# Performance work log

Hardware: AMD Instinct MI355X
Metric: run time of the kernel (lower is better)

Reference implementation:

```python
import jax, jax.numpy as jnp
import numpy as np

B, S, D = 8, 1024, 128
EPS = 1e-7
LN_EPS = 1e-3  # keras LayerNormalization default


def setup_inputs() -> dict:
    key = jax.random.key(0)
    ks = jax.random.split(key, 8)
    sd = 1.0 / np.sqrt(D)
    return {
        "x": jax.random.normal(ks[0], (B, S, D), jnp.float32),
        "Wq": jax.random.normal(ks[1], (D, D), jnp.float32) * sd,
        "bq": jnp.zeros((D,), jnp.float32),
        "Wm": jax.random.normal(ks[2], (D, D), jnp.float32) * sd,
        "bm": jnp.zeros((D,), jnp.float32),
        "Ww": jax.random.normal(ks[3], (D, 1), jnp.float32) * sd,
        "bw": jnp.zeros((1,), jnp.float32),
        "Wc": jax.random.normal(ks[4], (D, 1), jnp.float32) * sd,
        "bc": jnp.zeros((1,), jnp.float32),
        "emb_map": jax.random.normal(ks[5], (D, D, D), jnp.float32) * 0.02,
        "gamma": jnp.ones((D,), jnp.float32),
        "beta": jnp.zeros((D,), jnp.float32),
    }


def reference(x, Wq, bq, Wm, bm, Ww, bw, Wc, bc, emb_map, gamma, beta):
    b_, s_, d_ = x.shape
    q = x @ Wq + bq                      # [B,S,D]
    m = jax.nn.sigmoid(x @ Wm + bm)      # [B,S,D]
    w = jax.nn.relu(x @ Ww + bw)         # [B,S,1]
    c = jax.nn.relu(x @ Wc + bc)         # [B,S,1]

    # distances: for query pos i, preceding pos j (j<i) has distance i-j
    idx = jnp.arange(s_)
    dist = (idx[:, None] - idx[None, :]).astype(x.dtype)   # [S,S]
    valid = dist > 0                                       # strict causal
    # cosh positional decay, zero outside causal window -> [B,S,S]
    pe = jnp.where(valid[None], 1.0 / jnp.cosh((dist[None] - c) / (w + EPS)), 0.0)

    # angle between (pe * x_j * m_i + eps) and (q_i + eps), expanded analytically
    qp = q + EPS
    t1 = jnp.einsum('bjd,bid->bij', x, m * qp)             # sum_d x_j m_i q'_i
    s1 = jnp.einsum('bjd,bid->bij', x, m)                  # sum_d x_j m_i
    s2 = jnp.einsum('bjd,bid->bij', x * x, m * m)          # sum_d (x_j m_i)^2
    dot = pe * t1 + EPS * jnp.sum(qp, axis=-1)[:, :, None]
    na = jnp.sqrt(pe * pe * s2 + 2.0 * EPS * pe * s1 + d_ * EPS * EPS)
    nb = jnp.linalg.norm(qp, axis=-1)[:, :, None]
    cos = jnp.where(valid[None], dot / (na * nb), 0.0)
    angle = jnp.where(valid[None], jnp.arccos(cos), 0.0)   # [B,S,S]

    # query_result_i = sum_j pe*angle * x_j  -> [B,S,D]
    qr = jnp.einsum('bij,bjd->bid', pe * angle, x)

    # embedding matrix: current_token (rows) outer query_result (cols),
    # contracted against rank-3 map: out[b,s,d] = sum_{j,k} x[b,s,j] qr[b,s,k] map[d,j,k]
    em = jnp.einsum('bsj,bsk->bsjk', x, qr).reshape(b_, s_, d_ * d_)
    mapped = em @ emb_map.reshape(d_, d_ * d_).T           # [B,S,D]

    res = mapped + x
    mu = jnp.mean(res, axis=-1, keepdims=True)
    var = jnp.var(res, axis=-1, keepdims=True)
    out = (res - mu) / jnp.sqrt(var + LN_EPS) * gamma + beta
    return out  # dropout is identity at inference
```

## Files before the change

### kernel.cpp

```cpp
#include <hip/hip_runtime.h>
#include <hip/hip_bf16.h>
#include <math.h>

#define DD 128
#define SS 1024
#define NROWS 8192
#define EPSF 1e-7f
#define LN_EPSF 1e-3f
#define TCUT 30.0f

typedef __attribute__((ext_vector_type(8))) short bf16x8;
typedef __attribute__((ext_vector_type(8))) _Float16 f16x8;
typedef __attribute__((ext_vector_type(4))) float f32x4;
typedef __attribute__((ext_vector_type(16))) float f32x16;

__device__ __forceinline__ void gload_lds16(const void* g, void* l) {
    __builtin_amdgcn_global_load_lds(
        (const __attribute__((address_space(1))) unsigned int*)g,
        (__attribute__((address_space(3))) unsigned int*)l, 16, 0, 0);
}
__device__ __forceinline__ short f2bf(float v) {
    union { __hip_bfloat16 h; short s; } u;
    u.h = __float2bfloat16(v);
    return u.s;
}
__device__ __forceinline__ float bf2f(short s) {
    union { __hip_bfloat16 h; short s; } u; u.s = s;
    return __bfloat162float(u.h);
}
__device__ __forceinline__ short f2h(float v) {
    union { _Float16 h; short s; } u;
    u.h = (_Float16)v;
    return u.s;
}
__device__ __forceinline__ unsigned int pkmul_f16(unsigned int a, unsigned int b) {
    unsigned int r;
    asm("v_pk_mul_f16 %0, %1, %2" : "=v"(r) : "v"(a), "v"(b));
    return r;
}
__device__ __forceinline__ unsigned int f2h_dup(float v) {
    union { _Float16 h[2]; unsigned int u; } c;
    c.h[0] = (_Float16)v; c.h[1] = c.h[0];
    return c.u;
}
__device__ __forceinline__ unsigned int pack_bf16(float lo, float hi) {
    unsigned int r;
    asm("v_cvt_pk_bf16_f32 %0, %1, %2" : "=v"(r) : "v"(lo), "v"(hi));
    return r;
}

__global__ __launch_bounds__(256) void k0a_emb(const float* __restrict__ emb,
                                               short* __restrict__ embB) {
    __shared__ float lt[128][132];
    int j = blockIdx.x, t = threadIdx.x;
    {
        int d = t >> 1, kh = (t & 1) * 64;
        const float* src = emb + (size_t)d * 16384 + (size_t)j * 128 + kh;
#pragma unroll
        for (int q = 0; q < 16; ++q)
            *(float4*)&lt[d][kh + q * 4] = *(const float4*)(src + q * 4);
    }
    __syncthreads();
#pragma unroll
    for (int i = 0; i < 8; ++i) {
        int idx = i * 256 + t;
        int l = idx & 63, s = (idx >> 6) & 7, dt = (idx >> 9) & 3;
        const float* p = &lt[dt * 32 + (l & 31)][s * 16 + (l >> 5) * 8];
        union { bf16x8 v; short sa[8]; } ob;
#pragma unroll
        for (int e = 0; e < 8; ++e) ob.sa[e] = f2h(p[e]);
        *(bf16x8*)(embB + (size_t)j * 16384 + dt * 4096 + s * 512 + (size_t)l * 8) = ob.v;
    }
}

__global__ __launch_bounds__(256) void k0w_split(const float* __restrict__ Wq,
        const float* __restrict__ Wm, short* __restrict__ Wfrag) {
    int T = blockIdx.x * 256 + threadIdx.x;
    int e = T & 7, l = (T >> 3) & 63, ks = (T >> 9) & 3, nt = (T >> 11) & 7,
        mat = (T >> 14) & 1;
    int k = ks * 32 + ((l >> 4) & 3) * 8 + e;
    int c = nt * 16 + (l & 15);
    float v = (mat ? Wm : Wq)[k * 128 + c];
    short h = f2bf(v);
    float lo = v - bf2f(h);
    Wfrag[((((size_t)(mat * 2 + 0) * 8 + nt) * 4 + ks) * 64 + l) * 8 + e] = h;
    Wfrag[((((size_t)(mat * 2 + 1) * 8 + nt) * 4 + ks) * 64 + l) * 8 + e] = f2bf(lo);
}

__global__ __launch_bounds__(256) void k0c_xsplit(const float* __restrict__ x,
        const float* __restrict__ Ww, const float* __restrict__ bw,
        const float* __restrict__ Wc, const float* __restrict__ bc,
        short* __restrict__ xh2, short* __restrict__ xl2,
        float* __restrict__ scal) {
    __shared__ float xs[32][129];
    int rb = blockIdx.x, t = threadIdx.x;
    {
        int r = t >> 3, d0 = (t & 7) * 16;
        const float4* src = (const float4*)(x + (size_t)(rb * 32 + r) * 128 + d0);
#pragma unroll
        for (int q = 0; q < 4; ++q) *(float4*)&xs[r][d0 + q * 4] = src[q];
    }
    __syncthreads();
    int ks = (t >> 5) & 3, rf = t >> 7, l0 = (t & 31) * 2;
    union { bf16x8 v[2]; short s[16]; } hb, lb;
#pragma unroll
    for (int li = 0; li < 2; ++li) {
        int l = l0 + li;
        const float* p = &xs[rf * 16 + (l & 15)][ks * 32 + ((l >> 4) & 3) * 8];
#pragma unroll
        for (int e = 0; e < 8; ++e) {
            float v = p[e];
            short h = f2bf(v);
            hb.s[li * 8 + e] = h;
            lb.s[li * 8 + e] = f2bf(v - bf2f(h));
        }
    }
    {
        short* d1 = xh2 + (size_t)rb * 4096 + (size_t)t * 16;
        short* d2 = xl2 + (size_t)rb * 4096 + (size_t)t * 16;
        *(bf16x8*)d1 = hb.v[0]; *(bf16x8*)(d1 + 8) = hb.v[1];
        *(bf16x8*)d2 = lb.v[0]; *(bf16x8*)(d2 + 8) = lb.v[1];
    }
    int rr = t >> 3, seg = t & 7;
    float pw = 0.f, pc = 0.f;
#pragma unroll
    for (int dq = 0; dq < 16; ++dq) {
        float xv = xs[rr][seg * 16 + dq];
        pw = fmaf(xv, Ww[seg * 16 + dq], pw);
        pc = fmaf(xv, Wc[seg * 16 + dq], pc);
    }
    pw += __shfl_xor(pw, 1); pw += __shfl_xor(pw, 2); pw += __shfl_xor(pw, 4);
    pc += __shfl_xor(pc, 1); pc += __shfl_xor(pc, 2); pc += __shfl_xor(pc, 4);
    if (seg == 0) {
        scal[(size_t)(rb * 32 + rr) * 4 + 0] = fmaxf(pw + bw[0], 0.f);
        scal[(size_t)(rb * 32 + rr) * 4 + 1] = fmaxf(pc + bc[0], 0.f);
    }
}

__global__ __launch_bounds__(256) void k1_mfma(
    const short* __restrict__ xh2, const short* __restrict__ xl2,
    const short* __restrict__ Wfrag,
    const float* __restrict__ bq, const float* __restrict__ bm,
    float* __restrict__ mq, float* __restrict__ mo, float* __restrict__ scal)
{
    __shared__ __align__(16) short wl[65536];
    __shared__ float red[32][4][2];
    int t = threadIdx.x, w = t >> 6, l = t & 63;
    int l15 = l & 15, g = l >> 4;
    int row0 = blockIdx.x * 32;
#pragma unroll
    for (int it = 0; it < 32; ++it)
        gload_lds16(Wfrag + (size_t)(it * 256 + t) * 8, wl + (size_t)(it * 256 + w * 64) * 8);
    const short* xb  = xh2 + (size_t)blockIdx.x * 4096;
    const short* xlb = xl2 + (size_t)blockIdx.x * 4096;
    bf16x8 Ah[2][4], Al[2][4];
#pragma unroll
    for (int rf = 0; rf < 2; ++rf)
#pragma unroll
        for (int ks = 0; ks < 4; ++ks) {
            size_t o = ((size_t)(rf * 4 + ks) * 64 + l) * 8;
            Ah[rf][ks] = *(const bf16x8*)(xb + o);
            Al[rf][ks] = *(const bf16x8*)(xlb + o);
        }
    __syncthreads();
    f32x4 accq[2][2] = {}, accm[2][2] = {};
#pragma unroll
    for (int ntp = 0; ntp < 2; ++ntp) {
        int nt = w * 2 + ntp;
#pragma unroll
        for (int ks = 0; ks < 4; ++ks) {
            bf16x8 bhq = *(const bf16x8*)(wl + ((size_t)(0  + nt) * 4 + ks) * 512 + l * 8);
            bf16x8 blq = *(const bf16x8*)(wl + ((size_t)(8  + nt) * 4 + ks) * 512 + l * 8);
            bf16x8 bhm = *(const bf16x8*)(wl + ((size_t)(16 + nt) * 4 + ks) * 512 + l * 8);
            bf16x8 blm = *(const bf16x8*)(wl + ((size_t)(24 + nt) * 4 + ks) * 512 + l * 8);
#pragma unroll
            for (int rf = 0; rf < 2; ++rf) {
                accq[rf][ntp] = __builtin_amdgcn_mfma_f32_16x16x32_bf16(Ah[rf][ks], bhq, accq[rf][ntp], 0, 0, 0);
                accq[rf][ntp] = __builtin_amdgcn_mfma_f32_16x16x32_bf16(Ah[rf][ks], blq, accq[rf][ntp], 0, 0, 0);
                accq[rf][ntp] = __builtin_amdgcn_mfma_f32_16x16x32_bf16(Al[rf][ks], bhq, accq[rf][ntp], 0, 0, 0);
                accm[rf][ntp] = __builtin_amdgcn_mfma_f32_16x16x32_bf16(Ah[rf][ks], bhm, accm[rf][ntp], 0, 0, 0);
                accm[rf][ntp] = __builtin_amdgcn_mfma_f32_16x16x32_bf16(Ah[rf][ks], blm, accm[rf][ntp], 0, 0, 0);
                accm[rf][ntp] = __builtin_amdgcn_mfma_f32_16x16x32_bf16(Al[rf][ks], bhm, accm[rf][ntp], 0, 0, 0);
            }
        }
    }
    float sq1[2][4] = {{0,0,0,0},{0,0,0,0}};
    float sq2[2][4] = {{0,0,0,0},{0,0,0,0}};
#pragma unroll
    for (int ntp = 0; ntp < 2; ++ntp) {
        int c = (w * 2 + ntp) * 16 + l15;
        float bqv = bq[c] + EPSF, bmv = bm[c];
#pragma unroll
        for (int rf = 0; rf < 2; ++rf)
#pragma unroll
            for (int reg = 0; reg < 4; ++reg) {
                int rloc = rf * 16 + g * 4 + reg;
                float qp = accq[rf][ntp][reg] + bqv;
                float mv = 1.0f / (1.0f + expf(-(accm[rf][ntp][reg] + bmv)));
                size_t o = (size_t)(row0 + rloc) * 128 + c;
                mq[o] = mv * qp;
                mo[o] = mv;
                sq1[rf][reg] += qp;
                sq2[rf][reg] += qp * qp;
            }
    }
#pragma unroll
    for (int rf = 0; rf < 2; ++rf)
#pragma unroll
        for (int reg = 0; reg < 4; ++reg) {
            float a = sq1[rf][reg], b = sq2[rf][reg];
            a += __shfl_xor(a, 1); a += __shfl_xor(a, 2);
            a += __shfl_xor(a, 4); a += __shfl_xor(a, 8);
            b += __shfl_xor(b, 1); b += __shfl_xor(b, 2);
            b += __shfl_xor(b, 4); b += __shfl_xor(b, 8);
            if (l15 == 0) {
                red[rf * 16 + g * 4 + reg][w][0] = a;
                red[rf * 16 + g * 4 + reg][w][1] = b;
            }
        }
    __syncthreads();
    if (t < 32) {
        float a = red[t][0][0] + red[t][1][0] + red[t][2][0] + red[t][3][0];
        float b = red[t][0][1] + red[t][1][1] + red[t][2][1] + red[t][3][1];
        scal[(size_t)(row0 + t) * 4 + 2] = a;
        scal[(size_t)(row0 + t) * 4 + 3] = sqrtf(b);
    }
}

__global__ __launch_bounds__(256) void k2_qr(
    const float* __restrict__ x,
    const float* __restrict__ mq, const float* __restrict__ mo,
    const float* __restrict__ scal, short* __restrict__ qrh2)
{
    int row = blockIdx.x;
    int i = row & (SS - 1);
    const float* xb = x + (size_t)(row - i) * DD;
    int t = threadIdx.x, w = t >> 6, l = t & 63;
    int sub = l >> 4, q = l & 15;
    int qo = q * 8;

    float mqv[8], mov[8];
    {
        const float* mp = mq + (size_t)row * DD + qo;
        float4 a = *(const float4*)mp, b = *(const float4*)(mp + 4);
        mqv[0] = a.x; mqv[1] = a.y; mqv[2] = a.z; mqv[3] = a.w;
        mqv[4] = b.x; mqv[5] = b.y; mqv[6] = b.z; mqv[7] = b.w;
        const float* op = mo + (size_t)row * DD + qo;
        float4 c = *(const float4*)op, d = *(const float4*)(op + 4);
        mov[0] = c.x; mov[1] = c.y; mov[2] = c.z; mov[3] = c.w;
        mov[4] = d.x; mov[5] = d.y; mov[6] = d.z; mov[7] = d.w;
    }
    float wv = scal[row * 4 + 0], cv = scal[row * 4 + 1];
    float sumqp = scal[row * 4 + 2], nb = scal[row * 4 + 3];
    float wi = wv + EPSF;
    float dmaxf = cv + TCUT * wi;
    int dmax = (dmaxf >= (float)i) ? i : (int)dmaxf;

    float acc[8] = {0.f, 0.f, 0.f, 0.f, 0.f, 0.f, 0.f, 0.f};
    int nit = (dmax + 15) >> 4;
    int dbase = 1 + w * 4 + sub;
    for (int it = 0; it < nit; ++it) {
        int dist = dbase + it * 16;
        float xv[8];
        if (dist <= dmax) {
            const float* xp = xb + (size_t)(i - dist) * DD + qo;
            float4 a = *(const float4*)xp, b = *(const float4*)(xp + 4);
            xv[0] = a.x; xv[1] = a.y; xv[2] = a.z; xv[3] = a.w;
            xv[4] = b.x; xv[5] = b.y; xv[6] = b.z; xv[7] = b.w;
        } else {
#pragma unroll
            for (int e = 0; e < 8; ++e) xv[e] = 0.f;
        }
        float t1 = 0.f, s1 = 0.f, s2 = 0.f;
#pragma unroll
        for (int e = 0; e < 8; ++e) {
            float xm = xv[e] * mov[e];
            t1 = fmaf(xv[e], mqv[e], t1);
            s1 += xm;
            s2 = fmaf(xm, xm, s2);
        }
#pragma unroll
        for (int off = 1; off < 16; off <<= 1) {
            t1 += __shfl_xor(t1, off);
            s1 += __shfl_xor(s1, off);
            s2 += __shfl_xor(s2, off);
        }
        float tt = ((float)dist - cv) / wi;
        float pe = 1.0f / coshf(tt);
        float dotv = fmaf(pe, t1, EPSF * sumqp);
        float na = sqrtf(fmaf(pe * pe, s2,
                         fmaf(2.0f * EPSF * pe, s1, (float)DD * EPSF * EPSF)));
        float cosv = fminf(1.0f, fmaxf(-1.0f, dotv / (na * nb)));
        float ang = acosf(cosv);
        float wgt = pe * ang;
#pragma unroll
        for (int e = 0; e < 8; ++e) acc[e] = fmaf(wgt, xv[e], acc[e]);
    }
#pragma unroll
    for (int e = 0; e < 8; ++e) {
        acc[e] += __shfl_xor(acc[e], 16);
        acc[e] += __shfl_xor(acc[e], 32);
    }
    __shared__ float sq[4][DD];
    if (l < 16) {
#pragma unroll
        for (int e = 0; e < 8; ++e) sq[w][qo + e] = acc[e];
    }
    __syncthreads();
    if (t < DD) {
        float v = sq[0][t] + sq[1][t] + sq[2][t] + sq[3][t];
        int rbq = row >> 7, rr = row & 127, rt2 = rr >> 5, lp = rr & 31;
        int k = t;
        qrh2[(((size_t)(rbq * 4 + rt2) * 8 + (k >> 4)) * 64
              + (lp + 32 * ((k >> 3) & 1))) * 8 + (k & 7)] = f2h(v);
    }
}

__global__ __launch_bounds__(256, 2) void k3_gemm(
    const float* __restrict__ x, const short* __restrict__ embB,
    const short* __restrict__ qrh2, short* __restrict__ partb)
{
    __shared__ __align__(16) short bB[2][16384];
    __shared__ unsigned int xtd[16][132];
    int t = threadIdx.x, w = t >> 6, l = t & 63;
    int l31 = l & 31, hi = l >> 5;
    int rh = w >> 1, dh = w & 1;
    int rb = blockIdx.x, js = blockIdx.y;

    {
        int r = t >> 1, jq = (t & 1) * 8;
        const float* xp = x + (size_t)(rb * 128 + r) * 128 + js * 16 + jq;
        float4 a = *(const float4*)xp, b = *(const float4*)(xp + 4);
        xtd[jq + 0][r] = f2h_dup(a.x); xtd[jq + 1][r] = f2h_dup(a.y);
        xtd[jq + 2][r] = f2h_dup(a.z); xtd[jq + 3][r] = f2h_dup(a.w);
        xtd[jq + 4][r] = f2h_dup(b.x); xtd[jq + 5][r] = f2h_dup(b.y);
        xtd[jq + 6][r] = f2h_dup(b.z); xtd[jq + 7][r] = f2h_dup(b.w);
    }

    {
        const short* src = embB + (size_t)(js * 16) * 16384;
#pragma unroll
        for (int i = 0; i < 8; ++i)
            gload_lds16(src + (size_t)(i * 256 + t) * 8,
                        &bB[0][0] + (size_t)(i * 256 + w * 64) * 8);
    }

    unsigned int qrp[2][8][4];
#pragma unroll
    for (int rt = 0; rt < 2; ++rt) {
        int R32 = rb * 4 + rh * 2 + rt;
#pragma unroll
        for (int s = 0; s < 8; ++s) {
            union { f16x8 v; unsigned int u[4]; } qb;
            qb.v = *(const f16x8*)(qrh2 + (((size_t)R32 * 8 + s) * 64 + l) * 8);
#pragma unroll
            for (int p = 0; p < 4; ++p) qrp[rt][s][p] = qb.u[p];
        }
    }

    f32x16 acc[2][2];
#pragma unroll
    for (int rt = 0; rt < 2; ++rt)
#pragma unroll
        for (int i = 0; i < 2; ++i)
#pragma unroll
            for (int q = 0; q < 16; ++q) acc[rt][i][q] = 0.f;

    __syncthreads();

#pragma unroll 1
    for (int jj = 0; jj < 16; ++jj) {
        int cur = jj & 1;
        if (jj < 15) {
            const short* src = embB + (size_t)(js * 16 + jj + 1) * 16384;
#pragma unroll
            for (int i = 0; i < 8; ++i)
                gload_lds16(src + (size_t)(i * 256 + t) * 8,
                            &bB[cur ^ 1][0] + (size_t)(i * 256 + w * 64) * 8);
        }
        unsigned int xs0 = xtd[jj][rh * 64 + l31];
        unsigned int xs1 = xtd[jj][rh * 64 + 32 + l31];
        const short* bb = &bB[cur][0] + (size_t)(dh * 2) * 4096 + (size_t)l * 8;
#pragma unroll
        for (int s = 0; s < 8; ++s) {
            f16x8 Bd0 = *(const f16x8*)(bb + s * 512);
            f16x8 Bd1 = *(const f16x8*)(bb + 4096 + s * 512);
            union { f16x8 v; unsigned int u[4]; } a0, a1;
#pragma unroll
            for (int p = 0; p < 4; ++p) {
                a0.u[p] = pkmul_f16(qrp[0][s][p], xs0);
                a1.u[p] = pkmul_f16(qrp[1][s][p], xs1);
            }
            acc[0][0] = __builtin_amdgcn_mfma_f32_32x32x16_f16(a0.v, Bd0, acc[0][0], 0, 0, 0);
            acc[0][1] = __builtin_amdgcn_mfma_f32_32x32x16_f16(a0.v, Bd1, acc[0][1], 0, 0, 0);
            acc[1][0] = __builtin_amdgcn_mfma_f32_32x32x16_f16(a1.v, Bd0, acc[1][0], 0, 0, 0);
            acc[1][1] = __builtin_amdgcn_mfma_f32_32x32x16_f16(a1.v, Bd1, acc[1][1], 0, 0, 0);
        }
        __syncthreads();
    }

    short* sofh = &bB[0][0];
#pragma unroll
    for (int rt = 0; rt < 2; ++rt)
#pragma unroll
        for (int i = 0; i < 2; ++i)
#pragma unroll
            for (int q = 0; q < 16; ++q) {
                int r = rh * 64 + rt * 32 + (q & 3) + 8 * (q >> 2) + 4 * hi;
                int c = dh * 64 + i * 32 + l31;
                sofh[r * 136 + c] = f2h(0.f), sofh[r * 136 + c] = f2bf(acc[rt][i][q]);
            }
    __syncthreads();
    size_t pbase = (size_t)js * ((size_t)NROWS * DD);
#pragma unroll
    for (int i = 0; i < 8; ++i) {
        int idx = i * 256 + t;
        int r = idx >> 4, c8 = (idx & 15) * 8;
        *(bf16x8*)(partb + pbase + (size_t)(rb * 128 + r) * 128 + c8)
            = *(const bf16x8*)(sofh + r * 136 + c8);
    }
}

__global__ __launch_bounds__(256) void k4_ln(
    const float* __restrict__ x, const short* __restrict__ partb,
    const float* __restrict__ gamma, const float* __restrict__ beta,
    float* __restrict__ out)
{
    int wave = threadIdx.x >> 6, lane = threadIdx.x & 63;
    int row = blockIdx.x * 4 + wave;
    size_t base = (size_t)row * DD;
    float r0 = x[base + lane], r1 = x[base + lane + 64];
#pragma unroll
    for (int p = 0; p < 8; ++p) {
        r0 += bf2f(partb[(size_t)p * 1048576 + base + lane]);
        r1 += bf2f(partb[(size_t)p * 1048576 + base + lane + 64]);
    }
    float s = r0 + r1, s2 = r0 * r0 + r1 * r1;
#pragma unroll
    for (int off = 32; off > 0; off >>= 1) {
        s += __shfl_xor(s, off);
        s2 += __shfl_xor(s2, off);
    }
    float mu = s * (1.0f / DD);
    float var = s2 * (1.0f / DD) - mu * mu;
    var = fmaxf(var, 0.0f);
    float rs = rsqrtf(var + LN_EPSF);
    out[base + lane] = (r0 - mu) * rs * gamma[lane] + beta[lane];
    out[base + lane + 64] = (r1 - mu) * rs * gamma[lane + 64] + beta[lane + 64];
}

extern "C" void kernel_launch(void* const* d_in, const int* in_sizes, int n_in,
                              void* d_out, int out_size, void* d_ws, size_t ws_size,
                              hipStream_t stream) {
    const float* x     = (const float*)d_in[0];
    const float* Wq    = (const float*)d_in[1];
    const float* bq    = (const float*)d_in[2];
    const float* Wm    = (const float*)d_in[3];
    const float* bm    = (const float*)d_in[4];
    const float* Ww    = (const float*)d_in[5];
    const float* bw    = (const float*)d_in[6];
    const float* Wc    = (const float*)d_in[7];
    const float* bc    = (const float*)d_in[8];
    const float* emb   = (const float*)d_in[9];
    const float* gamma = (const float*)d_in[10];
    const float* beta  = (const float*)d_in[11];
    float* out = (float*)d_out;
    float* ws  = (float*)d_ws;

    short* embB  = (short*)ws;
    short* qrh2  = (short*)(ws + 1048576);
    float* scal  = ws + 1572864;
    short* partb = (short*)(ws + 1605632);
    float* tr    = ws + 1605632;
    short* xh2   = (short*)tr;
    short* xl2   = (short*)(tr + 524288);
    float* mq    = tr + 1048576;
    float* mo    = tr + 2097152;
    short* Wfrag = (short*)(tr + 3145728);

    hipLaunchKernelGGL(k0a_emb,   dim3(128),    dim3(256), 0, stream, emb, embB);
    hipLaunchKernelGGL(k0w_split, dim3(256),    dim3(256), 0, stream, Wq, Wm, Wfrag);
    hipLaunchKernelGGL(k0c_xsplit,dim3(256),    dim3(256), 0, stream,
                       x, Ww, bw, Wc, bc, xh2, xl2, scal);
    hipLaunchKernelGGL(k1_mfma,   dim3(256),    dim3(256), 0, stream,
                       xh2, xl2, Wfrag, bq, bm, mq, mo, scal);
    hipLaunchKernelGGL(k2_qr,     dim3(8192),   dim3(256), 0, stream,
                       x, mq, mo, scal, qrh2);
    hipLaunchKernelGGL(k3_gemm,   dim3(64, 8),  dim3(256), 0, stream,
                       x, embB, qrh2, partb);
    hipLaunchKernelGGL(k4_ln,     dim3(2048),   dim3(256), 0, stream,
                       x, partb, gamma, beta, out);
}
```

Baseline: 87.98 us.

## Fuse x split into MFMA kernel, widen emb prep grid, vectorize layernorm

Removes the separate x bf16 hi/lo split kernel. k1_mfma now loads x into LDS, builds the A fragments and computes the w/c scalars in place, which saves one launch and a round trip of the split arrays through global memory. The embedding-map conversion is split across 4x more blocks to use more CUs. The layernorm kernel uses float4/ushort4 vector loads with 8 rows per block, and a redundant LDS store is dropped. The cost is more LDS use in k1, which could lower its occupancy.

New measurement: 84.23 us. 4.3% less time.

```diff
diff --git a/kernel.cpp b/kernel.cpp
--- a/kernel.cpp
+++ b/kernel.cpp
@@ -43,34 +43,31 @@
     c.h[0] = (_Float16)v; c.h[1] = c.h[0];
     return c.u;
 }
-__device__ __forceinline__ unsigned int pack_bf16(float lo, float hi) {
-    unsigned int r;
-    asm("v_cvt_pk_bf16_f32 %0, %1, %2" : "=v"(r) : "v"(lo), "v"(hi));
-    return r;
-}
 
 __global__ __launch_bounds__(256) void k0a_emb(const float* __restrict__ emb,
                                                short* __restrict__ embB) {
-    __shared__ float lt[128][132];
-    int j = blockIdx.x, t = threadIdx.x;
-    {
-        int d = t >> 1, kh = (t & 1) * 64;
-        const float* src = emb + (size_t)d * 16384 + (size_t)j * 128 + kh;
-#pragma unroll
-        for (int q = 0; q < 16; ++q)
-            *(float4*)&lt[d][kh + q * 4] = *(const float4*)(src + q * 4);
-    }
-    __syncthreads();
-#pragma unroll
-    for (int i = 0; i < 8; ++i) {
-        int idx = i * 256 + t;
-        int l = idx & 63, s = (idx >> 6) & 7, dt = (idx >> 9) & 3;
-        const float* p = &lt[dt * 32 + (l & 31)][s * 16 + (l >> 5) * 8];
-        union { bf16x8 v; short sa[8]; } ob;
-#pragma unroll
-        for (int e = 0; e < 8; ++e) ob.sa[e] = f2h(p[e]);
-        *(bf16x8*)(embB + (size_t)j * 16384 + dt * 4096 + s * 512 + (size_t)l * 8) = ob.v;
-    }
+    __shared__ float lt[32][132];
+    int j = blockIdx.x, dt = blockIdx.y, t = threadIdx.x;
+    {
+        int dl = t >> 3, k0 = (t & 7) * 16;
+        const float* src = emb + (size_t)(dt * 32 + dl) * 16384 + (size_t)j * 128 + k0;
+#pragma unroll
+        for (int q = 0; q < 4; ++q)
+            *(float4*)&lt[dl][k0 + q * 4] = *(const float4*)(src + q * 4);
+    }
+    __syncthreads();
+    int s = t >> 5, l0 = (t & 31) * 2;
+    union { bf16x8 v[2]; short sa[16]; } ob;
+#pragma unroll
+    for (int li = 0; li < 2; ++li) {
+        int l = l0 + li;
+        const float* p = &lt[l & 31][s * 16 + (l >> 5) * 8];
+#pragma unroll
+        for (int e = 0; e < 8; ++e) ob.sa[li * 8 + e] = f2h(p[e]);
+    }
+    short* dst = embB + (size_t)j * 16384 + dt * 4096 + s * 512 + (size_t)l0 * 8;
+    *(bf16x8*)dst = ob.v[0];
+    *(bf16x8*)(dst + 8) = ob.v[1];
 }
 
 __global__ __launch_bounds__(256) void k0w_split(const float* __restrict__ Wq,
@@ -87,63 +84,15 @@
     Wfrag[((((size_t)(mat * 2 + 1) * 8 + nt) * 4 + ks) * 64 + l) * 8 + e] = f2bf(lo);
 }
 
-__global__ __launch_bounds__(256) void k0c_xsplit(const float* __restrict__ x,
-        const float* __restrict__ Ww, const float* __restrict__ bw,
-        const float* __restrict__ Wc, const float* __restrict__ bc,
-        short* __restrict__ xh2, short* __restrict__ xl2,
-        float* __restrict__ scal) {
-    __shared__ float xs[32][129];
-    int rb = blockIdx.x, t = threadIdx.x;
-    {
-        int r = t >> 3, d0 = (t & 7) * 16;
-        const float4* src = (const float4*)(x + (size_t)(rb * 32 + r) * 128 + d0);
-#pragma unroll
-        for (int q = 0; q < 4; ++q) *(float4*)&xs[r][d0 + q * 4] = src[q];
-    }
-    __syncthreads();
-    int ks = (t >> 5) & 3, rf = t >> 7, l0 = (t & 31) * 2;
-    union { bf16x8 v[2]; short s[16]; } hb, lb;
-#pragma unroll
-    for (int li = 0; li < 2; ++li) {
-        int l = l0 + li;
-        const float* p = &xs[rf * 16 + (l & 15)][ks * 32 + ((l >> 4) & 3) * 8];
-#pragma unroll
-        for (int e = 0; e < 8; ++e) {
-            float v = p[e];
-            short h = f2bf(v);
-            hb.s[li * 8 + e] = h;
-            lb.s[li * 8 + e] = f2bf(v - bf2f(h));
-        }
-    }
-    {
-        short* d1 = xh2 + (size_t)rb * 4096 + (size_t)t * 16;
-        short* d2 = xl2 + (size_t)rb * 4096 + (size_t)t * 16;
-        *(bf16x8*)d1 = hb.v[0]; *(bf16x8*)(d1 + 8) = hb.v[1];
-        *(bf16x8*)d2 = lb.v[0]; *(bf16x8*)(d2 + 8) = lb.v[1];
-    }
-    int rr = t >> 3, seg = t & 7;
-    float pw = 0.f, pc = 0.f;
-#pragma unroll
-    for (int dq = 0; dq < 16; ++dq) {
-        float xv = xs[rr][seg * 16 + dq];
-        pw = fmaf(xv, Ww[seg * 16 + dq], pw);
-        pc = fmaf(xv, Wc[seg * 16 + dq], pc);
-    }
-    pw += __shfl_xor(pw, 1); pw += __shfl_xor(pw, 2); pw += __shfl_xor(pw, 4);
-    pc += __shfl_xor(pc, 1); pc += __shfl_xor(pc, 2); pc += __shfl_xor(pc, 4);
-    if (seg == 0) {
-        scal[(size_t)(rb * 32 + rr) * 4 + 0] = fmaxf(pw + bw[0], 0.f);
-        scal[(size_t)(rb * 32 + rr) * 4 + 1] = fmaxf(pc + bc[0], 0.f);
-    }
-}
-
 __global__ __launch_bounds__(256) void k1_mfma(
-    const short* __restrict__ xh2, const short* __restrict__ xl2,
-    const short* __restrict__ Wfrag,
+    const float* __restrict__ x, const short* __restrict__ Wfrag,
     const float* __restrict__ bq, const float* __restrict__ bm,
+    const float* __restrict__ Ww, const float* __restrict__ bw,
+    const float* __restrict__ Wc, const float* __restrict__ bc,
     float* __restrict__ mq, float* __restrict__ mo, float* __restrict__ scal)
 {
     __shared__ __align__(16) short wl[65536];
+    __shared__ float xs[32][129];
     __shared__ float red[32][4][2];
     int t = threadIdx.x, w = t >> 6, l = t & 63;
     int l15 = l & 15, g = l >> 4;
@@ -151,18 +100,48 @@
 #pragma unroll
     for (int it = 0; it < 32; ++it)
         gload_lds16(Wfrag + (size_t)(it * 256 + t) * 8, wl + (size_t)(it * 256 + w * 64) * 8);
-    const short* xb  = xh2 + (size_t)blockIdx.x * 4096;
-    const short* xlb = xl2 + (size_t)blockIdx.x * 4096;
+    {
+        int r = t >> 3, d0 = (t & 7) * 16;
+        const float4* src = (const float4*)(x + (size_t)(row0 + r) * 128 + d0);
+#pragma unroll
+        for (int q = 0; q < 4; ++q) *(float4*)&xs[r][d0 + q * 4] = src[q];
+    }
+    __syncthreads();
+
     bf16x8 Ah[2][4], Al[2][4];
 #pragma unroll
     for (int rf = 0; rf < 2; ++rf)
 #pragma unroll
         for (int ks = 0; ks < 4; ++ks) {
-            size_t o = ((size_t)(rf * 4 + ks) * 64 + l) * 8;
-            Ah[rf][ks] = *(const bf16x8*)(xb + o);
-            Al[rf][ks] = *(const bf16x8*)(xlb + o);
-        }
-    __syncthreads();
+            union { bf16x8 v; short sa[8]; } ah, al;
+#pragma unroll
+            for (int e = 0; e < 8; ++e) {
+                float v = xs[rf * 16 + l15][ks * 32 + g * 8 + e];
+                short h = f2bf(v);
+                ah.sa[e] = h;
+                al.sa[e] = f2bf(v - bf2f(h));
+            }
+            Ah[rf][ks] = ah.v;
+            Al[rf][ks] = al.v;
+        }
+
+    {
+        int rr = t >> 3, seg = t & 7;
+        float pw = 0.f, pc = 0.f;
+#pragma unroll
+        for (int dq = 0; dq < 16; ++dq) {
+            float xv = xs[rr][seg * 16 + dq];
+            pw = fmaf(xv, Ww[seg * 16 + dq], pw);
+            pc = fmaf(xv, Wc[seg * 16 + dq], pc);
+        }
+        pw += __shfl_xor(pw, 1); pw += __shfl_xor(pw, 2); pw += __shfl_xor(pw, 4);
+        pc += __shfl_xor(pc, 1); pc += __shfl_xor(pc, 2); pc += __shfl_xor(pc, 4);
+        if (seg == 0) {
+            scal[(size_t)(row0 + rr) * 4 + 0] = fmaxf(pw + bw[0], 0.f);
+            scal[(size_t)(row0 + rr) * 4 + 1] = fmaxf(pc + bc[0], 0.f);
+        }
+    }
+
     f32x4 accq[2][2] = {}, accm[2][2] = {};
 #pragma unroll
     for (int ntp = 0; ntp < 2; ++ntp) {
@@ -408,7 +387,7 @@
             for (int q = 0; q < 16; ++q) {
                 int r = rh * 64 + rt * 32 + (q & 3) + 8 * (q >> 2) + 4 * hi;
                 int c = dh * 64 + i * 32 + l31;
-                sofh[r * 136 + c] = f2h(0.f), sofh[r * 136 + c] = f2bf(acc[rt][i][q]);
+                sofh[r * 136 + c] = f2bf(acc[rt][i][q]);
             }
     __syncthreads();
     size_t pbase = (size_t)js * ((size_t)NROWS * DD);
@@ -426,18 +405,23 @@
     const float* __restrict__ gamma, const float* __restrict__ beta,
     float* __restrict__ out)
 {
-    int wave = threadIdx.x >> 6, lane = threadIdx.x & 63;
-    int row = blockIdx.x * 4 + wave;
-    size_t base = (size_t)row * DD;
-    float r0 = x[base + lane], r1 = x[base + lane + 64];
+    int t = threadIdx.x;
+    int rl = t >> 5, lane32 = t & 31;
+    int row = blockIdx.x * 8 + rl;
+    int c4 = lane32 * 4;
+    size_t base = (size_t)row * DD + c4;
+    float4 r = *(const float4*)(x + base);
 #pragma unroll
     for (int p = 0; p < 8; ++p) {
-        r0 += bf2f(partb[(size_t)p * 1048576 + base + lane]);
-        r1 += bf2f(partb[(size_t)p * 1048576 + base + lane + 64]);
-    }
-    float s = r0 + r1, s2 = r0 * r0 + r1 * r1;
-#pragma unroll
-    for (int off = 32; off > 0; off >>= 1) {
+        ushort4 u = *(const ushort4*)((const unsigned short*)partb
+                                      + (size_t)p * 1048576 + base);
+        r.x += bf2f((short)u.x); r.y += bf2f((short)u.y);
+        r.z += bf2f((short)u.z); r.w += bf2f((short)u.w);
+    }
+    float s = r.x + r.y + r.z + r.w;
+    float s2 = r.x * r.x + r.y * r.y + r.z * r.z + r.w * r.w;
+#pragma unroll
+    for (int off = 1; off < 32; off <<= 1) {
         s += __shfl_xor(s, off);
         s2 += __shfl_xor(s2, off);
     }
@@ -445,8 +429,14 @@
     float var = s2 * (1.0f / DD) - mu * mu;
     var = fmaxf(var, 0.0f);
     float rs = rsqrtf(var + LN_EPSF);
-    out[base + lane] = (r0 - mu) * rs * gamma[lane] + beta[lane];
-    out[base + lane + 64] = (r1 - mu) * rs * gamma[lane + 64] + beta[lane + 64];
+    float4 g = *(const float4*)(gamma + c4);
+    float4 b = *(const float4*)(beta + c4);
+    float4 o;
+    o.x = (r.x - mu) * rs * g.x + b.x;
+    o.y = (r.y - mu) * rs * g.y + b.y;
+    o.z = (r.z - mu) * rs * g.z + b.z;
+    o.w = (r.w - mu) * rs * g.w + b.w;
+    *(float4*)(out + base) = o;
 }
 
 extern "C" void kernel_launch(void* const* d_in, const int* in_sizes, int n_in,
@@ -472,22 +462,18 @@
     float* scal  = ws + 1572864;
     short* partb = (short*)(ws + 1605632);
     float* tr    = ws + 1605632;
-    short* xh2   = (short*)tr;
-    short* xl2   = (short*)(tr + 524288);
     float* mq    = tr + 1048576;
     float* mo    = tr + 2097152;
     short* Wfrag = (short*)(tr + 3145728);
 
-    hipLaunchKernelGGL(k0a_emb,   dim3(128),    dim3(256), 0, stream, emb, embB);
+    hipLaunchKernelGGL(k0a_emb,   dim3(128, 4), dim3(256), 0, stream, emb, embB);
     hipLaunchKernelGGL(k0w_split, dim3(256),    dim3(256), 0, stream, Wq, Wm, Wfrag);
-    hipLaunchKernelGGL(k0c_xsplit,dim3(256),    dim3(256), 0, stream,
-                       x, Ww, bw, Wc, bc, xh2, xl2, scal);
     hipLaunchKernelGGL(k1_mfma,   dim3(256),    dim3(256), 0, stream,
-                       xh2, xl2, Wfrag, bq, bm, mq, mo, scal);
+                       x, Wfrag, bq, bm, Ww, bw, Wc, bc, mq, mo, scal);
     hipLaunchKernelGGL(k2_qr,     dim3(8192),   dim3(256), 0, stream,
                        x, mq, mo, scal, qrh2);
     hipLaunchKernelGGL(k3_gemm,   dim3(64, 8),  dim3(256), 0, stream,
                        x, embB, qrh2, partb);
-    hipLaunchKernelGGL(k4_ln,     dim3(2048),   dim3(256), 0, stream,
+    hipLaunchKernelGGL(k4_ln,     dim3(1024),   dim3(256), 0, stream,
                        x, partb, gamma, beta, out);
 }
```
